# Optimization experiments

Measured on AMD Instinct MI355X. Metric: run time of the kernel, lower is better.

## Reference

```python
import jax, jax.numpy as jnp
import numpy as np

H = 1024          # hidden_size (hardcoded in module)
NB = 32           # nbones
D = 3 * NB        # 96 pose features
T_IN = 49         # input_window_size - 1 encoder steps
T_OUT = 25        # output_window_size
B = 512


def setup_inputs() -> dict:
    key = jax.random.key(0)
    ks = jax.random.split(key, 12)
    s = 1.0 / np.sqrt(H)  # PyTorch GRUCell default init scale
    u = lambda k, shape, sc: jax.random.uniform(k, shape, jnp.float32, -sc, sc)
    return {
        "encoder_inputs": jax.random.normal(ks[0], (B, T_IN, D), jnp.float32),
        "decoder_inputs": jax.random.normal(ks[1], (B, 1, D), jnp.float32),
        "enc_Wih": u(ks[2], (3 * H, D), s),
        "enc_Whh": u(ks[3], (3 * H, H), s),
        "enc_bih": u(ks[4], (3 * H,), s),
        "enc_bhh": u(ks[5], (3 * H,), s),
        "dec_Wih": u(ks[6], (3 * H, D), s),
        "dec_Whh": u(ks[7], (3 * H, H), s),
        "dec_bih": u(ks[8], (3 * H,), s),
        "dec_bhh": u(ks[9], (3 * H,), s),
        "W_out": u(ks[10], (H, D), 0.04),   # module inits uniform(-0.04, 0.04)
        "b_out": u(ks[11], (D,), 0.04),
    }


def gru_cell(x, h, Wih, Whh, bih, bhh):
    # PyTorch nn.GRUCell: gates ordered (r, z, n)
    gi = x @ Wih.T + bih          # [B, 3H]
    gh = h @ Whh.T + bhh          # [B, 3H]
    gir, giz, gin = jnp.split(gi, 3, axis=-1)
    ghr, ghz, ghn = jnp.split(gh, 3, axis=-1)
    r = jax.nn.sigmoid(gir + ghr)
    z = jax.nn.sigmoid(giz + ghz)
    n = jnp.tanh(gin + r * ghn)
    return (1.0 - z) * n + z * h


def reference(encoder_inputs, decoder_inputs,
              enc_Wih, enc_Whh, enc_bih, enc_bhh,
              dec_Wih, dec_Whh, dec_bih, dec_bhh,
              W_out, b_out):
    b = encoder_inputs.shape[0]
    dt = encoder_inputs.dtype

    # --- encoder: sequential GRU over T_IN frames (result unused by decoder,
    # faithfully matching the original module, which never consumes enc_state) ---
    def enc_step(h, x):
        return gru_cell(x, h, enc_Wih, enc_Whh, enc_bih, enc_bhh), None

    enc_state, _ = jax.lax.scan(enc_step, jnp.zeros((b, H), dt),
                                jnp.swapaxes(encoder_inputs, 0, 1))

    # first hidden is zeros (PyTorch GRUCell default when h not given) ---
    p = decoder_inputs[:, 0, :]

    def dec_step(carry, _):
        h, x = carry
        hn = gru_cell(x, h, dec_Wih, dec_Whh, dec_bih, dec_bhh)
        out = hn @ W_out + b_out
        return (hn, out), out

    _, outs = jax.lax.scan(dec_step, (jnp.zeros((b, H), dt), p),
                           None, length=T_OUT)
    prediction = jnp.swapaxes(outs, 0, 1)  # [B, T_OUT, D]
    return prediction
```

## Files before the change

### kernel.cpp

```cpp
#include <hip/hip_runtime.h>
#include <hip/hip_bf16.h>

typedef __attribute__((ext_vector_type(8))) short short8;
typedef __attribute__((ext_vector_type(4))) float f32x4;
typedef __attribute__((ext_vector_type(4))) unsigned u32x4;
typedef unsigned short u16;

#define BB 512
#define HH 1024
#define TT 25
#define CTB 128
#define HSZ (BB*HH)


__device__ __forceinline__ float sigm(float x){ return 1.f/(1.f+__expf(-x)); }
__device__ __forceinline__ float tanh_(float x){
  float e = __expf(-2.f*fabsf(x));
  float t = (1.f-e)/(1.f+e);
  return copysignf(t, x);
}
__device__ __forceinline__ u16 f2bf(float x){
  union { float f; unsigned u; } v; v.f = x;
  unsigned r = v.u + 0x7FFFu + ((v.u>>16)&1u);
  return (u16)(r>>16);
}
__device__ __forceinline__ void store16_wt(void* p, u32x4 v){
  asm volatile("global_store_dwordx4 %0, %1, off sc0 sc1" :: "v"(p), "v"(v) : "memory");
}
__device__ __forceinline__ void aload(short8 &d, const short8* p){
  asm volatile("global_load_dwordx4 %0, %1, off" : "=v"(d) : "v"(p));
}

#if __has_builtin(__builtin_amdgcn_global_load_lds)
#define GLOAD_LDS16(g, l) __builtin_amdgcn_global_load_lds( \
    (const __attribute__((address_space(1))) void*)(g), \
    (__attribute__((address_space(3))) void*)(l), 16, 0, 0)
#define HAVE_GLL 1
#else
#define HAVE_GLL 0
#endif

__device__ __forceinline__ size_t wc_idx(int ct, int r, int k){
  int nf = r>>4, rl = r&15, kit = k>>5, k31 = k&31;
  int lane = rl | (((k31>>3)&3)<<4);
  return (size_t)ct*49152 + ((size_t)(kit*3+nf)*64 + (size_t)lane)*8 + (k31&7);
}


__device__ void prep_wx_body(int bid, float* smem,
                             const float* __restrict__ Wih,
                             const float* __restrict__ Wout,
                             u16* __restrict__ Wcp){
  float (*sWih)[97] = (float(*)[97])smem;
  float (*sWo)[97]  = (float(*)[97])(smem + 32*97);
  int tid = threadIdx.x;
  int nt = bid % 96, kt = bid / 96;
  for (int i = tid; i < 32*96; i += 256){ int r2=i/96, d=i%96; sWih[r2][d] = Wih[(size_t)(nt*32+r2)*96 + d]; }
  for (int i = tid; i < 64*96; i += 256){ int r2=i/96, d=i%96; sWo[r2][d]  = Wout[(size_t)(kt*64+r2)*96 + d]; }
  __syncthreads();
  int ni = tid & 31, kb = tid >> 5;
  float acc[8];
  #pragma unroll
  for (int i=0;i<8;i++) acc[i]=0.f;
  for (int d = 0; d < 96; d++){
    float a = sWih[ni][d];
    #pragma unroll
    for (int i=0;i<8;i++) acc[i] += a * sWo[kb*8 + i][d];
  }
  int n = nt*32 + ni;
  int g = n >> 10, j = n & 1023;
  int ct = j >> 3, u = j & 7, r = g*8 + u;
  size_t base = wc_idx(ct, r, kt*64 + kb*8);
  #pragma unroll
  for (int i=0;i<8;i++) Wcp[base+i] = f2bf(acc[i]);
}

__device__ void prep_cast_body(int bid,
                               const float* __restrict__ Whh, const float* __restrict__ bhh,
                               const float* __restrict__ Wout,
                               u16* __restrict__ Wcp, float* __restrict__ cbias,
                               u16* __restrict__ WoT){
  int tid = threadIdx.x;
  if (bid < 3072){
    int g1 = bid >> 10, j = bid & 1023;
    int ct = j >> 3, u = j & 7, r = (3+g1)*8 + u;
    const float* src = Whh + (size_t)bid*1024;
    if (tid < 128){
      int k0 = tid*8;
      size_t base = wc_idx(ct, r, k0);
      #pragma unroll
      for (int i=0;i<8;i++) Wcp[base+i] = f2bf(src[k0+i]);
    }
    if (!tid) cbias[ct*48 + r] = bhh[bid];
  } else {
    int d = bid - 3072;
    for (int k = tid; k < 1024; k += 256)
      WoT[(size_t)d*1024 + k] = f2bf(Wout[(size_t)k*96 + d]);
  }
}

__device__ void prep_cx_body(int bid,
                             const float* __restrict__ Wih, const float* __restrict__ bih,
                             const float* __restrict__ bout, float* __restrict__ cbias){
  int n = bid*256 + threadIdx.x;
  if (n >= 3072) return;
  float acc = bih[n];
  const float* wrow = Wih + (size_t)n*96;
  for (int d = 0; d < 96; d++) acc += bout[d]*wrow[d];
  int g = n >> 10, j = n & 1023;
  cbias[(j>>3)*48 + g*8 + (j&7)] = acc;
}

__device__ void step0_body(int bid, float* smem,
                           const float* __restrict__ dec_in, const float* __restrict__ Wih,
                           const float* __restrict__ bih, const float* __restrict__ bhh,
                           float* __restrict__ h_f32, u16* __restrict__ h_bf,
                           unsigned* __restrict__ flags){
  if (bid == 0 && threadIdx.x < 256) flags[threadIdx.x] = 0u;
  float (*sP)[97] = (float(*)[97])smem;
  float (*sW)[97] = (float(*)[97])(smem + 64*97);
  int tid = threadIdx.x;
  int bt = bid & 7;
  int jt = bid >> 3;
  for (int i = tid; i < 64*96; i += 256){ int r=i/96, d=i%96; sP[r][d] = dec_in[(size_t)(bt*64+r)*96 + d]; }
  int tb = tid >> 4, tj = tid & 15;
  float gg[3][4][4];
  for (int g = 0; g < 3; g++){
    __syncthreads();
    for (int i = tid; i < 64*96; i += 256){ int r=i/96, d=i%96; sW[r][d] = Wih[((size_t)g*1024 + jt*64 + r)*96 + d]; }
    __syncthreads();
    float acc[4][4];
    #pragma unroll
    for (int x=0;x<4;x++)
      #pragma unroll
      for (int y=0;y<4;y++) acc[x][y]=0.f;
    for (int d = 0; d < 96; d++){
      float a[4], wv[4];
      #pragma unroll
      for (int x=0;x<4;x++) a[x]  = sP[tb + x*16][d];
      #pragma unroll
      for (int y=0;y<4;y++) wv[y] = sW[tj + y*16][d];
      #pragma unroll
      for (int x=0;x<4;x++)
        #pragma unroll
        for (int y=0;y<4;y++) acc[x][y] += a[x]*wv[y];
    }
    #pragma unroll
    for (int x=0;x<4;x++)
      #pragma unroll
      for (int y=0;y<4;y++) gg[g][x][y] = acc[x][y];
  }
  #pragma unroll
  for (int x=0;x<4;x++)
    #pragma unroll
    for (int y=0;y<4;y++){
      int b = bt*64 + tb + x*16;
      int j = jt*64 + tj + y*16;
      float gir = gg[0][x][y] + bih[j];
      float giz = gg[1][x][y] + bih[1024+j];
      float gin = gg[2][x][y] + bih[2048+j];
      float r = sigm(gir + bhh[j]);
      float z = sigm(giz + bhh[1024+j]);
      float nn = tanh_(gin + r*bhh[2048+j]);
      float h = (1.f - z)*nn;
      h_f32[(size_t)j*512 + b] = h;
      h_bf[(size_t)(((b>>4)*32 + (j>>5))*512 + (b&15)*32 + (j&31))] = f2bf(h);
    }
}

__global__ __launch_bounds__(256)
void k_prep_all(const float* __restrict__ dec_in,
                const float* __restrict__ Wih, const float* __restrict__ Whh,
                const float* __restrict__ bih, const float* __restrict__ bhh,
                const float* __restrict__ Wout, const float* __restrict__ bout,
                u16* __restrict__ Wcp, float* __restrict__ cbias,
                u16* __restrict__ WoT,
                float* __restrict__ hf0, u16* __restrict__ hb0,
                unsigned* __restrict__ flags){
  __shared__ float smem[2*64*97];
  int bid = blockIdx.x;
  if (bid < 1536)            prep_wx_body(bid, smem, Wih, Wout, Wcp);
  else if (bid < 4704)       prep_cast_body(bid-1536, Whh, bhh, Wout, Wcp, cbias, WoT);
  else if (bid < 4716)       prep_cx_body(bid-4704, Wih, bih, bout, cbias);
  else                       step0_body(bid-4716, smem, dec_in, Wih, bih, bhh, hf0, hb0, flags);
}

__global__ __launch_bounds__(1024, 1)
void k_persist10(const float* __restrict__ hf0, u16* __restrict__ hbase,
                 const u16* __restrict__ Wcp, const float* __restrict__ cbias,
                 unsigned* __restrict__ flags){
  __shared__ short8 sB[6144];
  __shared__ f32x4 sRed[8][2][3][64];
  int b = blockIdx.x, tid = threadIdx.x;
  int lane = tid & 63, w = tid >> 6;
  int l16 = lane & 15, lk = lane >> 4;
  int kh = w & 1, wr = w >> 1;
  int r8 = b & 7;
  int bt = r8 >> 2;
  int ct = (b >> 3)*4 + (r8 & 3);

  const short8* Wblk = (const short8*)Wcp + (size_t)ct*6144;
#if HAVE_GLL
  #pragma unroll
  for (int it = 0; it < 6; it++){
    int i = it*1024 + tid;
    GLOAD_LDS16(Wblk + i, &sB[i]);
  }
#else
  for (int i = tid; i < 6144; i += 1024) sB[i] = Wblk[i];
#endif

  float c0 = cbias[ct*48 +  0 + l16];
  float c1 = cbias[ct*48 + 16 + l16];
  float c2 = cbias[ct*48 + 32 + l16];
  bool hiB = (l16 & 8) != 0;
  int rowA = bt*256 + wr*32;
  int rb0 = rowA >> 4;
  int myFlag = bt*128 + ct;
  const int gk0 = kh*16;
  const int other = kh ^ 1;
  const bool kh0 = (kh == 0);

  float hold[4];
  if (!hiB){
    int colg = ct*8 + l16;
    f32x4 h4 = *(const f32x4*)(hf0 + (size_t)colg*512 + rowA + kh*16 + lk*4);
    hold[0]=h4[0]; hold[1]=h4[1]; hold[2]=h4[2]; hold[3]=h4[3];
  }
  __syncthreads();

  for (int t = 1; t <= 24; ++t){
    const short8* pin8 = (const short8*)(hbase + (size_t)(t-1)*HSZ);
    u16* pout = hbase + (size_t)t*HSZ;
    const short8* Ap = pin8 + (size_t)rb0*2048 + l16*4 + lk;

    short8 ar[4][2];
    #define AISSUE(k, s) { \
      aload(ar[s][0], Ap + 0*2048 + (size_t)(k)*64); \
      aload(ar[s][1], Ap + 1*2048 + (size_t)(k)*64); }

    AISSUE(gk0+0,0); AISSUE(gk0+1,1); AISSUE(gk0+2,2); AISSUE(gk0+3,3);

    short8 brw[2][3];
    #pragma unroll
    for (int nf = 0; nf < 3; nf++) brw[0][nf] = sB[gk0*192 + nf*64 + lane];

    f32x4 acc[2][3];
    #pragma unroll
    for (int m=0;m<2;m++)
      #pragma unroll
      for (int nf=0;nf<3;nf++) acc[m][nf] = f32x4{0.f,0.f,0.f,0.f};

    #pragma unroll
    for (int q = 0; q < 16; q++){
      const int cur = q & 1, nxt = cur ^ 1, sa = q & 3;
      if (q <= 12)      asm volatile("s_waitcnt vmcnt(6)" ::: "memory");
      else if (q == 13) asm volatile("s_waitcnt vmcnt(4)" ::: "memory");
      else if (q == 14) asm volatile("s_waitcnt vmcnt(2)" ::: "memory");
      else              asm volatile("s_waitcnt vmcnt(0)" ::: "memory");
      __builtin_amdgcn_sched_barrier(0);
      if (q < 15){
        #pragma unroll
        for (int nf = 0; nf < 3; nf++) brw[nxt][nf] = sB[(gk0+q+1)*192 + nf*64 + lane];
      }
      acc[0][0] = __builtin_amdgcn_mfma_f32_16x16x32_bf16(ar[sa][0], brw[cur][0], acc[0][0], 0,0,0);
      acc[1][0] = __builtin_amdgcn_mfma_f32_16x16x32_bf16(ar[sa][1], brw[cur][0], acc[1][0], 0,0,0);
      acc[0][1] = __builtin_amdgcn_mfma_f32_16x16x32_bf16(ar[sa][0], brw[cur][1], acc[0][1], 0,0,0);
      acc[1][1] = __builtin_amdgcn_mfma_f32_16x16x32_bf16(ar[sa][1], brw[cur][1], acc[1][1], 0,0,0);
      acc[0][2] = __builtin_amdgcn_mfma_f32_16x16x32_bf16(ar[sa][0], brw[cur][2], acc[0][2], 0,0,0);
      acc[1][2] = __builtin_amdgcn_mfma_f32_16x16x32_bf16(ar[sa][1], brw[cur][2], acc[1][2], 0,0,0);
      if (q < 12) AISSUE(gk0+q+4, sa);
    }
    #undef AISSUE

    #pragma unroll
    for (int nf = 0; nf < 3; nf++)
      sRed[wr][kh][nf][lane] = kh0 ? acc[1][nf] : acc[0][nf];
    __syncthreads();
    f32x4 own[3];
    #pragma unroll
    for (int nf = 0; nf < 3; nf++)
      own[nf] = (kh0 ? acc[0][nf] : acc[1][nf]) + sRed[wr][other][nf][lane];

    {
      #pragma unroll
      for (int j=0;j<4;j++){
        float g0 = own[0][j] + c0;
        float g1 = own[1][j] + c1;
        float g2 = own[2][j] + c2;
        float v1 = hiB ? g1 : g2;
        float w1 = __shfl_xor(v1, 8, 64);
        float rz = sigm(g0 + w1);
        float w2 = __shfl_xor(rz, 8, 64);
        float v3 = hiB ? (w2 * g2) : 0.f;
        float w3 = __shfl_xor(v3, 8, 64);
        float hnew = 0.f;
        if (!hiB){
          float nn = tanh_(g1 + w3);
          hnew = (1.f - w2)*nn + w2*hold[j];
          hold[j] = hnew;
        }
        float o1 = __shfl_xor(hnew, 1, 64);
        unsigned pk = ((unsigned)f2bf(o1) << 16) | (unsigned)f2bf(hnew);
        unsigned pk2 = __shfl_xor(pk, 2, 64);
        unsigned q2 = __shfl_xor(pk, 4, 64);
        unsigned q3 = __shfl_xor(pk2, 4, 64);
        if (l16 == 0){
          u32x4 vv = {pk, pk2, q2, q3};
          store16_wt((char*)pout + (size_t)(rb0+kh)*32768 + (size_t)(ct>>2)*1024
                                 + (size_t)(lk*4+j)*64 + (size_t)(ct&3)*16, vv);
        }
      }
    }

    __syncthreads();
    if (tid == 0)
      __hip_atomic_store(&flags[myFlag], (unsigned)t,
                         __ATOMIC_RELAXED, __HIP_MEMORY_SCOPE_AGENT);
    if (tid < 128){
      unsigned tgt = (unsigned)t;
      while (__hip_atomic_load(&flags[bt*128 + tid], __ATOMIC_RELAXED,
                               __HIP_MEMORY_SCOPE_AGENT) < tgt)
        __builtin_amdgcn_s_sleep(2);
    }
    __syncthreads();
  }
}

__global__ __launch_bounds__(384)
void k_pred(const u16* __restrict__ hbase, const u16* __restrict__ WoT,
            const float* __restrict__ bout, float* __restrict__ pred){
  int blk = blockIdx.x;
  int i = blk >> 5, rbt = blk & 31;
  int tid = threadIdx.x;
  int lane = tid & 63, bn = tid >> 6;
  int l16 = lane & 15, lk = lane >> 4;
  const short8* Aq = (const short8*)(hbase + (size_t)i*HSZ)
                     + (size_t)rbt*2048 + l16*4 + lk;
  const short8* Bq = (const short8*)WoT + (size_t)(bn*16 + l16)*128 + lk;
  f32x4 acc = {0.f,0.f,0.f,0.f};
  #pragma unroll 8
  for (int kit = 0; kit < 32; kit++)
    acc = __builtin_amdgcn_mfma_f32_16x16x32_bf16(Aq[kit*64], Bq[kit*4], acc, 0,0,0);
  int c = bn*16 + l16;
  float bb = bout[c];
  #pragma unroll
  for (int j=0;j<4;j++){
    int row = rbt*16 + lk*4 + j;
    pred[(size_t)row*2400 + (size_t)i*96 + c] = acc[j] + bb;
  }
}

extern "C" void kernel_launch(void* const* d_in, const int* in_sizes, int n_in,
                              void* d_out, int out_size, void* d_ws, size_t ws_size,
                              hipStream_t stream){
  const float* dec_in = (const float*)d_in[1];
  const float* Wih  = (const float*)d_in[6];
  const float* Whh  = (const float*)d_in[7];
  const float* bih  = (const float*)d_in[8];
  const float* bhh  = (const float*)d_in[9];
  const float* Wout = (const float*)d_in[10];
  const float* bout = (const float*)d_in[11];
  float* pred = (float*)d_out;

  char* ws = (char*)d_ws;
  size_t off = 0;
  u16* Wcp = (u16*)(ws + off);   off += (size_t)CTB*48*1024*2;
  u16* WoT = (u16*)(ws + off);   off += (size_t)96*1024*2;
  float* cbias = (float*)(ws + off); off += (size_t)6144*4;
  off = (off + 255) & ~(size_t)255;
  float* hf0 = (float*)(ws + off); off += (size_t)BB*HH*4;
  u16* hbase = (u16*)(ws + off);   off += (size_t)TT*HSZ*2;
  off = (off + 255) & ~(size_t)255;
  unsigned* flags = (unsigned*)(ws + off); off += 1024;

  k_prep_all<<<4844, 256, 0, stream>>>(dec_in, Wih, Whh, bih, bhh, Wout, bout,
                                       Wcp, cbias, WoT, hf0, hbase, flags);

  const float* hf0_c = hf0;
  void* kargs[] = {(void*)&hf0_c, (void*)&hbase, (void*)&Wcp, (void*)&cbias,
                   (void*)&flags};
  hipLaunchCooperativeKernel((const void*)k_persist10, dim3(256), dim3(1024),
                             kargs, 0, stream);

  k_pred<<<800, 384, 0, stream>>>(hbase, WoT, bout, pred);
}
```

Before: 454.8 us.

## Fuse output projection into persistent GRU kernel using idle wait time

Removes the separate prediction kernel. Inside the persistent recurrent kernel, 12 waves of the first 96 column blocks compute the output projection for the previous step's hidden state while waiting on the inter-block flag barrier, reduce the partial sums in shared memory, and write pred. The last step's projection runs after the loop. This saves a kernel launch and overlaps the projection with synchronisation stalls, at the cost of extra MFMA and memory traffic inside the critical recurrent loop.

```diff
diff --git a/kernel.cpp b/kernel.cpp
--- a/kernel.cpp
+++ b/kernel.cpp
@@ -186,11 +186,13 @@
 }
 
 __global__ __launch_bounds__(1024, 1)
-void k_persist10(const float* __restrict__ hf0, u16* __restrict__ hbase,
+void k_persist12(const float* __restrict__ hf0, u16* __restrict__ hbase,
                  const u16* __restrict__ Wcp, const float* __restrict__ cbias,
-                 unsigned* __restrict__ flags){
+                 const u16* __restrict__ WoT, const float* __restrict__ bout,
+                 float* __restrict__ pred, unsigned* __restrict__ flags){
   __shared__ short8 sB[6144];
   __shared__ f32x4 sRed[8][2][3][64];
+  __shared__ f32x4 sPred[6][2][64];
   int b = blockIdx.x, tid = threadIdx.x;
   int lane = tid & 63, w = tid >> 6;
   int l16 = lane & 15, lk = lane >> 4;
@@ -220,6 +222,9 @@
   const int gk0 = kh*16;
   const int other = kh ^ 1;
   const bool kh0 = (kh == 0);
+  const bool doPredBlk = (ct < 96);
+  const int bm = ct / 6;
+  const int predFrag = bt*16 + bm;
 
   float hold[4];
   if (!hiB){
@@ -317,6 +322,18 @@
     if (tid == 0)
       __hip_atomic_store(&flags[myFlag], (unsigned)t,
                          __ATOMIC_RELAXED, __HIP_MEMORY_SCOPE_AGENT);
+    if (doPredBlk && w >= 2 && w < 14){
+      int pw = w - 2, pbn = pw % 6, pk2 = pw / 6;
+      const short8* Aq = pin8 + (size_t)predFrag*2048 + l16*4 + lk;
+      const short8* Bq = (const short8*)WoT + (size_t)(pbn*16 + l16)*128 + lk;
+      f32x4 accp = {0.f,0.f,0.f,0.f};
+      #pragma unroll 4
+      for (int q2 = 0; q2 < 16; q2++){
+        int kit = pk2*16 + q2;
+        accp = __builtin_amdgcn_mfma_f32_16x16x32_bf16(Aq[(size_t)kit*64], Bq[kit*4], accp, 0,0,0);
+      }
+      sPred[pbn][pk2][lane] = accp;
+    }
     if (tid < 128){
       unsigned tgt = (unsigned)t;
       while (__hip_atomic_load(&flags[bt*128 + tid], __ATOMIC_RELAXED,
@@ -324,30 +341,43 @@
         __builtin_amdgcn_s_sleep(2);
     }
     __syncthreads();
-  }
-}
-
-__global__ __launch_bounds__(384)
-void k_pred(const u16* __restrict__ hbase, const u16* __restrict__ WoT,
-            const float* __restrict__ bout, float* __restrict__ pred){
-  int blk = blockIdx.x;
-  int i = blk >> 5, rbt = blk & 31;
-  int tid = threadIdx.x;
-  int lane = tid & 63, bn = tid >> 6;
-  int l16 = lane & 15, lk = lane >> 4;
-  const short8* Aq = (const short8*)(hbase + (size_t)i*HSZ)
-                     + (size_t)rbt*2048 + l16*4 + lk;
-  const short8* Bq = (const short8*)WoT + (size_t)(bn*16 + l16)*128 + lk;
-  f32x4 acc = {0.f,0.f,0.f,0.f};
-  #pragma unroll 8
-  for (int kit = 0; kit < 32; kit++)
-    acc = __builtin_amdgcn_mfma_f32_16x16x32_bf16(Aq[kit*64], Bq[kit*4], acc, 0,0,0);
-  int c = bn*16 + l16;
-  float bb = bout[c];
-  #pragma unroll
-  for (int j=0;j<4;j++){
-    int row = rbt*16 + lk*4 + j;
-    pred[(size_t)row*2400 + (size_t)i*96 + c] = acc[j] + bb;
+    if (doPredBlk && w < 6){
+      f32x4 s = sPred[w][0][lane] + sPred[w][1][lane];
+      int c = w*16 + l16;
+      float bb = bout[c];
+      #pragma unroll
+      for (int j=0;j<4;j++){
+        int row = bt*256 + bm*16 + lk*4 + j;
+        pred[(size_t)row*2400 + (size_t)(t-1)*96 + c] = s[j] + bb;
+      }
+    }
+  }
+
+  if (doPredBlk){
+    const short8* pin8 = (const short8*)(hbase + (size_t)24*HSZ);
+    if (w >= 2 && w < 14){
+      int pw = w - 2, pbn = pw % 6, pk2 = pw / 6;
+      const short8* Aq = pin8 + (size_t)predFrag*2048 + l16*4 + lk;
+      const short8* Bq = (const short8*)WoT + (size_t)(pbn*16 + l16)*128 + lk;
+      f32x4 accp = {0.f,0.f,0.f,0.f};
+      #pragma unroll 4
+      for (int q2 = 0; q2 < 16; q2++){
+        int kit = pk2*16 + q2;
+        accp = __builtin_amdgcn_mfma_f32_16x16x32_bf16(Aq[(size_t)kit*64], Bq[kit*4], accp, 0,0,0);
+      }
+      sPred[pbn][pk2][lane] = accp;
+    }
+    __syncthreads();
+    if (w < 6){
+      f32x4 s = sPred[w][0][lane] + sPred[w][1][lane];
+      int c = w*16 + l16;
+      float bb = bout[c];
+      #pragma unroll
+      for (int j=0;j<4;j++){
+        int row = bt*256 + bm*16 + lk*4 + j;
+        pred[(size_t)row*2400 + (size_t)24*96 + c] = s[j] + bb;
+      }
+    }
   }
 }
 
@@ -378,10 +408,9 @@
                                        Wcp, cbias, WoT, hf0, hbase, flags);
 
   const float* hf0_c = hf0;
+  const u16* WoT_c = WoT;
   void* kargs[] = {(void*)&hf0_c, (void*)&hbase, (void*)&Wcp, (void*)&cbias,
-                   (void*)&flags};
-  hipLaunchCooperativeKernel((const void*)k_persist10, dim3(256), dim3(1024),
+                   (void*)&WoT_c, (void*)&bout, (void*)&pred, (void*)&flags};
+  hipLaunchCooperativeKernel((const void*)k_persist12, dim3(256), dim3(1024),
                              kargs, 0, stream);
-
-  k_pred<<<800, 384, 0, stream>>>(hbase, WoT, bout, pred);
-}
+}
```

Result: slower. 633.3 us (+39.3%).
